# Optimization experiments

Measured on AMD Instinct MI355X. Metric: run time of the kernel, lower is better.

## Reference

```python
import jax, jax.numpy as jnp
import numpy as np

K_DIM = 1024
HEADS = 16
D_K = K_DIM // HEADS


def setup_inputs() -> dict:
    key = jax.random.key(0)
    ks = jax.random.split(key, 6)
    b, t, k = 4, 1024, K_DIM
    scale = 1.0 / np.sqrt(k)
    return {
        "x": jax.random.normal(ks[0], (b, t, k), dtype=jnp.float32),
        "Wq": jax.random.normal(ks[1], (k, k), dtype=jnp.float32) * scale,
        "Wk": jax.random.normal(ks[2], (k, k), dtype=jnp.float32) * scale,
        "Wv": jax.random.normal(ks[3], (k, k), dtype=jnp.float32) * scale,
        "Wo": jax.random.normal(ks[4], (k, k), dtype=jnp.float32) * scale,
        "bo": jax.random.normal(ks[5], (k,), dtype=jnp.float32) * 0.01,
    }


def reference(x, Wq, Wk, Wv, Wo, bo):
    b, t, k = x.shape
    h, d_k = HEADS, D_K
    # Linear(k,k) applies x @ W.T; project then split heads -> [b, h, t, d_k]
    Q = (x @ Wq.T).reshape(b, t, h, d_k).transpose(0, 2, 1, 3)
    Kh = (x @ Wk.T).reshape(b, t, h, d_k).transpose(0, 2, 1, 3)
    V = (x @ Wv.T).reshape(b, t, h, d_k).transpose(0, 2, 1, 3)
    scores = jnp.einsum("bhqd,bhkd->bhqk", Q, Kh) / jnp.sqrt(jnp.float32(d_k))
    attn = jax.nn.softmax(scores, axis=-1)
    out = jnp.einsum("bhqk,bhkd->bhqd", attn, V)
    out = out.transpose(0, 2, 1, 3).reshape(b, t, k)
    return out @ Wo.T + bo
```

## Files before the change

### kernel.cpp

```cpp
#include <hip/hip_runtime.h>
#include <hip/hip_bf16.h>

typedef __attribute__((ext_vector_type(4))) float f32x4;
typedef __attribute__((ext_vector_type(8))) short short8;

#define B_   4
#define T_   1024
#define H_   16
#define DK_  64
#define KDIM 1024

#define QSCALE 0.18033688011112042f

__device__ __forceinline__ unsigned short f2bf(float f){
  union { float f; unsigned int u; } a; a.f = f;
  unsigned int u = a.u;
  return (unsigned short)((u + 0x7FFFu + ((u >> 16) & 1u)) >> 16);
}

__device__ __forceinline__ unsigned short f2bf_rn(float f){
  union { __hip_bfloat16 h; unsigned short u; } cv;
  cv.h = __float2bfloat16(f);
  return cv.u;
}

__device__ __forceinline__ void gload16(const void* g, void* l){
  __builtin_amdgcn_global_load_lds(
      (const __attribute__((address_space(1))) unsigned int*)g,
      (__attribute__((address_space(3))) unsigned int*)l,
      16, 0, 0);
}

__global__ __launch_bounds__(256) void convert5(
    const float* __restrict__ x,  const float* __restrict__ wq,
    const float* __restrict__ wk, const float* __restrict__ wv,
    const float* __restrict__ wo,
    short* __restrict__ xb,  short* __restrict__ wqb,
    short* __restrict__ wkb, short* __restrict__ wvb, short* __restrict__ wob)
{
  int i = blockIdx.x * 256 + threadIdx.x;
  const float* s; short* d; int off;
  if (i < (1 << 20)) { s = x; d = xb; off = i; }
  else {
    int j = i - (1 << 20);
    int w = j >> 18;
    off = j & ((1 << 18) - 1);
    s = (w == 0) ? wq : (w == 1) ? wk : (w == 2) ? wv : wo;
    d = (w == 0) ? wqb : (w == 1) ? wkb : (w == 2) ? wvb : wob;
  }
  float4 v = ((const float4*)s)[off];
  ushort4 o;
  o.x = f2bf(v.x); o.y = f2bf(v.y); o.z = f2bf(v.z); o.w = f2bf(v.w);
  ((ushort4*)d)[off] = o;
}

__device__ __forceinline__ void gemm2_core(
    const short* __restrict__ A, const short* __restrict__ W,
    int m0, int n0, short* As, short* Bs, f32x4 acc[4][4])
{
  const int tid = threadIdx.x, wv = tid >> 6, lane = tid & 63;
  const int lr = lane & 15, lq = lane >> 4;
  const int wr = wv >> 1, wc = wv & 1;
  const int swz = (lr & 7) << 3;
  const int r8 = lane >> 3;
  const int c8 = ((lane & 7) * 8) ^ (r8 * 8);

#pragma unroll
  for (int m = 0; m < 4; ++m)
#pragma unroll
    for (int n = 0; n < 4; ++n) acc[m][n] = (f32x4){0.f, 0.f, 0.f, 0.f};

  auto stage = [&](int buf, int kt) {
    const int k0 = kt * 64;
#pragma unroll
    for (int i = 0; i < 4; ++i) {
      const int r = (wv * 4 + i) * 8 + r8;
      gload16(A + (size_t)(m0 + r) * KDIM + k0 + c8, As + buf * 8192 + (wv * 4 + i) * 512);
      gload16(W + (size_t)(n0 + r) * KDIM + k0 + c8, Bs + buf * 8192 + (wv * 4 + i) * 512);
    }
  };

  stage(0, 0);
  asm volatile("s_waitcnt vmcnt(0)" ::: "memory");
  __builtin_amdgcn_s_barrier();

  int buf = 0;
  for (int kt = 0; kt < 16; ++kt) {
    if (kt < 15) stage(buf ^ 1, kt + 1);
    const short* Ab = As + buf * 8192;
    const short* Bb = Bs + buf * 8192;
#pragma unroll
    for (int kk = 0; kk < 2; ++kk) {
      short8 af[4], bfv[4];
#pragma unroll
      for (int m = 0; m < 4; ++m)
        af[m] = *(const short8*)(Ab + (wr * 64 + m * 16 + lr) * 64 + ((kk * 32 + lq * 8) ^ swz));
#pragma unroll
      for (int n = 0; n < 4; ++n)
        bfv[n] = *(const short8*)(Bb + (wc * 64 + n * 16 + lr) * 64 + ((kk * 32 + lq * 8) ^ swz));
      __builtin_amdgcn_s_setprio(1);
#pragma unroll
      for (int m = 0; m < 4; ++m)
#pragma unroll
        for (int n = 0; n < 4; ++n)
          acc[m][n] = __builtin_amdgcn_mfma_f32_16x16x32_bf16(af[m], bfv[n], acc[m][n], 0, 0, 0);
      __builtin_amdgcn_s_setprio(0);
    }
    asm volatile("s_waitcnt vmcnt(0)" ::: "memory");
    __builtin_amdgcn_s_barrier();
    buf ^= 1;
  }
}

__global__ __launch_bounds__(256, 2) void gemm2_qkv(
    const short* __restrict__ xb,
    const short* __restrict__ Wqb, const short* __restrict__ Wkb, const short* __restrict__ Wvb,
    short* __restrict__ Qb, short* __restrict__ Kb, short* __restrict__ VTb)
{
  __shared__ __align__(16) short As[2 * 8192];
  __shared__ __align__(16) short Bs[2 * 8192];
  const int bid = blockIdx.x;
  const int wgid = (bid & 7) * 96 + (bid >> 3);
  const int mx = wgid / 24, inner = wgid % 24;
  const int wsel = inner >> 3;
  const int m0 = mx * 128, n0 = (inner & 7) * 128;
  const short* W = (wsel == 0) ? Wqb : (wsel == 1) ? Wkb : Wvb;

  f32x4 acc[4][4];
  gemm2_core(xb, W, m0, n0, As, Bs, acc);

  const int tid = threadIdx.x, lane = tid & 63, wv = tid >> 6;
  const int lr = lane & 15, lq = lane >> 4, wr = wv >> 1, wc = wv & 1;
  if (wsel < 2) {
    short* O = wsel ? Kb : Qb;
    const float sc = wsel ? 1.0f : QSCALE;
#pragma unroll
    for (int m = 0; m < 4; ++m)
#pragma unroll
      for (int n = 0; n < 4; ++n)
#pragma unroll
        for (int j = 0; j < 4; ++j) {
          int row = m0 + wr * 64 + m * 16 + lq * 4 + j;
          int col = n0 + wc * 64 + n * 16 + lr;
          O[(size_t)row * KDIM + col] = (short)f2bf(acc[m][n][j] * sc);
        }
  } else {
#pragma unroll
    for (int m = 0; m < 4; ++m)
#pragma unroll
      for (int n = 0; n < 4; ++n) {
        int row = m0 + wr * 64 + m * 16 + lq * 4;
        int col = n0 + wc * 64 + n * 16 + lr;
        int b = row >> 10, t = row & 1023, h = col >> 6, d = col & 63;
        ushort4 v;
        v.x = f2bf(acc[m][n][0]); v.y = f2bf(acc[m][n][1]);
        v.z = f2bf(acc[m][n][2]); v.w = f2bf(acc[m][n][3]);
        *(ushort4*)&VTb[(size_t)((b * 16 + h) * 64 + d) * 1024 + t] = v;
      }
  }
}

__global__ __launch_bounds__(256, 2) void gemm2_out(
    const short* __restrict__ AOb, const short* __restrict__ Wob,
    const float* __restrict__ bias, float* __restrict__ out)
{
  __shared__ __align__(16) short As[2 * 8192];
  __shared__ __align__(16) short Bs[2 * 8192];
  const int bid = blockIdx.x;
  const int wgid = (bid & 7) * 32 + (bid >> 3);
  const int mx = wgid >> 3, ny = wgid & 7;
  const int m0 = mx * 128, n0 = ny * 128;

  f32x4 acc[4][4];
  gemm2_core(AOb, Wob, m0, n0, As, Bs, acc);

  const int tid = threadIdx.x, lane = tid & 63, wv = tid >> 6;
  const int lr = lane & 15, lq = lane >> 4, wr = wv >> 1, wc = wv & 1;
#pragma unroll
  for (int m = 0; m < 4; ++m)
#pragma unroll
    for (int n = 0; n < 4; ++n) {
      int col = n0 + wc * 64 + n * 16 + lr;
      float bv = bias[col];
#pragma unroll
      for (int j = 0; j < 4; ++j) {
        int row = m0 + wr * 64 + m * 16 + lq * 4 + j;
        out[(size_t)row * KDIM + col] = acc[m][n][j] + bv;
      }
    }
}

__global__ __launch_bounds__(256) void attn_kern(
    const short* __restrict__ Qb, const short* __restrict__ Kb,
    const short* __restrict__ VTb, short* __restrict__ AOb)
{
  __shared__ __align__(16) short kl[2][64 * 64];
  __shared__ __align__(16) short vl[2][64 * 64];
  __shared__ __align__(16) short pl[4][16 * 64];
  const int flat = blockIdx.y * 16 + blockIdx.x;
  const int wg = (flat & 7) * 128 + (flat >> 3);
  const int bh = wg >> 4, b = bh >> 4, h = bh & 15;
  const int q0 = (wg & 15) * 64;
  const int tid = threadIdx.x, wv = tid >> 6, lane = tid & 63;
  const int lr = lane & 15, lq = lane >> 4;

  const short* Qrow = Qb + (size_t)(b * T_ + q0 + wv * 16 + lr) * KDIM + h * DK_;
  short8 qf0 = *(const short8*)(Qrow + lq * 8);
  short8 qf1 = *(const short8*)(Qrow + 32 + lq * 8);

  const short* Kbase = Kb + (size_t)(b * T_) * KDIM + h * DK_;
  const short* Vbase = VTb + (size_t)(bh * DK_) * 1024;

  const int srow = tid >> 3, scol = (tid & 7) * 8;

  auto stage = [&](int buf, int kv0) {
#pragma unroll
    for (int p = 0; p < 2; ++p) {
      const int r = p * 32 + srow;
      gload16(Kbase + (size_t)(kv0 + r) * KDIM + (scol ^ ((r & 7) << 3)),
              &kl[buf][p * 2048 + wv * 512]);
    }
#pragma unroll
    for (int p = 0; p < 2; ++p) {
      const int r = p * 32 + srow;
      gload16(Vbase + (size_t)r * 1024 + kv0 + (scol ^ ((r & 7) << 3)),
              &vl[buf][p * 2048 + wv * 512]);
    }
  };

  f32x4 oacc[4];
#pragma unroll
  for (int i = 0; i < 4; ++i) oacc[i] = (f32x4){0.f, 0.f, 0.f, 0.f};
  float m_r = -1e30f, l_r = 0.f;
  const int swq = (lr & 7) << 3;
  short* plw = pl[wv];

  int cur = 0;
  stage(0, 0);
  __syncthreads();

  for (int kt = 0; kt < 16; ++kt) {
    if (kt < 15) stage(cur ^ 1, (kt + 1) * 64);

    f32x4 s[4];
#pragma unroll
    for (int nt = 0; nt < 4; ++nt) {
      const int kr = nt * 16 + lr;
      const int sw = (kr & 7) << 3;
      short8 kf0 = *(const short8*)&kl[cur][kr * 64 + ((lq * 8) ^ sw)];
      short8 kf1 = *(const short8*)&kl[cur][kr * 64 + ((32 + lq * 8) ^ sw)];
      f32x4 z = (f32x4){0.f, 0.f, 0.f, 0.f};
      z = __builtin_amdgcn_mfma_f32_16x16x32_bf16(kf0, qf0, z, 0, 0, 0);
      s[nt] = __builtin_amdgcn_mfma_f32_16x16x32_bf16(kf1, qf1, z, 0, 0, 0);
    }

    float mx;
    {
      float a0 = fmaxf(fmaxf(s[0][0], s[0][1]), fmaxf(s[0][2], s[0][3]));
      float a1 = fmaxf(fmaxf(s[1][0], s[1][1]), fmaxf(s[1][2], s[1][3]));
      float a2 = fmaxf(fmaxf(s[2][0], s[2][1]), fmaxf(s[2][2], s[2][3]));
      float a3 = fmaxf(fmaxf(s[3][0], s[3][1]), fmaxf(s[3][2], s[3][3]));
      mx = fmaxf(fmaxf(a0, a1), fmaxf(a2, a3));
    }
    mx = fmaxf(mx, __shfl_xor(mx, 16));
    mx = fmaxf(mx, __shfl_xor(mx, 32));
    if (!__all(mx <= m_r + 8.f)) {
      const float mn = fmaxf(m_r, mx);
      const float al = exp2f(m_r - mn);
      l_r *= al;
#pragma unroll
      for (int nt = 0; nt < 4; ++nt)
#pragma unroll
        for (int j = 0; j < 4; ++j) oacc[nt][j] *= al;
      m_r = mn;
    }
    float rs = 0.f;
#pragma unroll
    for (int nt = 0; nt < 4; ++nt)
#pragma unroll
      for (int j = 0; j < 4; ++j) {
        float e = exp2f(s[nt][j] - m_r);
        s[nt][j] = e;
        rs += e;
      }
    rs += __shfl_xor(rs, 16);
    rs += __shfl_xor(rs, 32);
    l_r += rs;

#pragma unroll
    for (int nt = 0; nt < 4; ++nt) {
      f32x4 v = s[nt];
      ushort4 u;
      u.x = f2bf_rn(v[0]); u.y = f2bf_rn(v[1]);
      u.z = f2bf_rn(v[2]); u.w = f2bf_rn(v[3]);
      *(ushort4*)&plw[lr * 64 + ((nt * 16 + lq * 4) ^ swq)] = u;
    }
    asm volatile("s_waitcnt lgkmcnt(0)" ::: "memory");
    short8 pf0 = *(const short8*)&plw[lr * 64 + ((lq * 8) ^ swq)];
    short8 pf1 = *(const short8*)&plw[lr * 64 + ((32 + lq * 8) ^ swq)];
#pragma unroll
    for (int ntd = 0; ntd < 4; ++ntd) {
      const int vr = ntd * 16 + lr;
      const int sw = (vr & 7) << 3;
      short8 vf0 = *(const short8*)&vl[cur][vr * 64 + ((lq * 8) ^ sw)];
      short8 vf1 = *(const short8*)&vl[cur][vr * 64 + ((32 + lq * 8) ^ sw)];
      oacc[ntd] = __builtin_amdgcn_mfma_f32_16x16x32_bf16(vf0, pf0, oacc[ntd], 0, 0, 0);
      oacc[ntd] = __builtin_amdgcn_mfma_f32_16x16x32_bf16(vf1, pf1, oacc[ntd], 0, 0, 0);
    }
    __syncthreads();
    cur ^= 1;
  }

  const float inv = 1.0f / l_r;
#pragma unroll
  for (int nt = 0; nt < 4; ++nt) {
    ushort4 u;
    u.x = f2bf_rn(oacc[nt][0] * inv);
    u.y = f2bf_rn(oacc[nt][1] * inv);
    u.z = f2bf_rn(oacc[nt][2] * inv);
    u.w = f2bf_rn(oacc[nt][3] * inv);
    *(ushort4*)&AOb[(size_t)(b * T_ + q0 + wv * 16 + lr) * KDIM + h * DK_ + nt * 16 + lq * 4] = u;
  }
}

extern "C" void kernel_launch(void* const* d_in, const int* in_sizes, int n_in,
                              void* d_out, int out_size, void* d_ws, size_t ws_size,
                              hipStream_t stream) {
  const float* x  = (const float*)d_in[0];
  const float* Wq = (const float*)d_in[1];
  const float* Wk = (const float*)d_in[2];
  const float* Wv = (const float*)d_in[3];
  const float* Wo = (const float*)d_in[4];
  const float* bo = (const float*)d_in[5];

  short* ws = (short*)d_ws;
  short* xb  = ws;
  short* Wqb = ws + 4194304;
  short* Wkb = ws + 5242880;
  short* Wvb = ws + 6291456;
  short* Wob = ws + 7340032;
  short* Qb  = ws + 8388608;
  short* Kb  = ws + 12582912;
  short* VTb = ws + 16777216;
  short* AOb = ws + 20971520;

  convert5<<<8192, 256, 0, stream>>>(x, Wq, Wk, Wv, Wo, xb, Wqb, Wkb, Wvb, Wob);
  gemm2_qkv<<<768, 256, 0, stream>>>(xb, Wqb, Wkb, Wvb, Qb, Kb, VTb);
  attn_kern<<<dim3(16, 64), 256, 0, stream>>>(Qb, Kb, VTb, AOb);
  gemm2_out<<<256, 256, 0, stream>>>(AOb, Wob, bo, (float*)d_out);
}
```

Baseline: 186.9 us.

## Vectorize GEMM epilogue stores via swapped MFMA operands; double query rows per attention wave

The GEMM core is templated so that for Q/K and output projections the MFMA operands are swapped, making each lane hold 4 consecutive columns and allowing vectorized ushort4/float4 stores instead of scalar strided stores. The attention kernel now processes 32 query rows per wave (128 per block, 512 blocks), so every K/V tile loaded into LDS is reused twice, halving K/V global traffic per query. This raises register pressure (doubled accumulators and scores) and halves block count, which may reduce occupancy.

After: 189.5 us. No clear change (+1.4%).

```diff
diff --git a/kernel.cpp b/kernel.cpp
--- a/kernel.cpp
+++ b/kernel.cpp
@@ -54,6 +54,7 @@
   ((ushort4*)d)[off] = o;
 }
 
+template<bool SWAP>
 __device__ __forceinline__ void gemm2_core(
     const short* __restrict__ A, const short* __restrict__ W,
     int m0, int n0, short* As, short* Bs, f32x4 acc[4][4])
@@ -102,8 +103,12 @@
 #pragma unroll
       for (int m = 0; m < 4; ++m)
 #pragma unroll
-        for (int n = 0; n < 4; ++n)
-          acc[m][n] = __builtin_amdgcn_mfma_f32_16x16x32_bf16(af[m], bfv[n], acc[m][n], 0, 0, 0);
+        for (int n = 0; n < 4; ++n) {
+          if constexpr (SWAP)
+            acc[m][n] = __builtin_amdgcn_mfma_f32_16x16x32_bf16(bfv[n], af[m], acc[m][n], 0, 0, 0);
+          else
+            acc[m][n] = __builtin_amdgcn_mfma_f32_16x16x32_bf16(af[m], bfv[n], acc[m][n], 0, 0, 0);
+        }
       __builtin_amdgcn_s_setprio(0);
     }
     asm volatile("s_waitcnt vmcnt(0)" ::: "memory");
@@ -126,25 +131,29 @@
   const int m0 = mx * 128, n0 = (inner & 7) * 128;
   const short* W = (wsel == 0) ? Wqb : (wsel == 1) ? Wkb : Wvb;
 
-  f32x4 acc[4][4];
-  gemm2_core(xb, W, m0, n0, As, Bs, acc);
-
   const int tid = threadIdx.x, lane = tid & 63, wv = tid >> 6;
   const int lr = lane & 15, lq = lane >> 4, wr = wv >> 1, wc = wv & 1;
+
   if (wsel < 2) {
+    f32x4 acc[4][4];
+    gemm2_core<true>(xb, W, m0, n0, As, Bs, acc);
     short* O = wsel ? Kb : Qb;
     const float sc = wsel ? 1.0f : QSCALE;
 #pragma unroll
-    for (int m = 0; m < 4; ++m)
-#pragma unroll
-      for (int n = 0; n < 4; ++n)
-#pragma unroll
-        for (int j = 0; j < 4; ++j) {
-          int row = m0 + wr * 64 + m * 16 + lq * 4 + j;
-          int col = n0 + wc * 64 + n * 16 + lr;
-          O[(size_t)row * KDIM + col] = (short)f2bf(acc[m][n][j] * sc);
-        }
+    for (int m = 0; m < 4; ++m) {
+      const int row = m0 + wr * 64 + m * 16 + lr;
+#pragma unroll
+      for (int n = 0; n < 4; ++n) {
+        const int colb = n0 + wc * 64 + n * 16 + lq * 4;
+        ushort4 u;
+        u.x = f2bf(acc[m][n][0] * sc); u.y = f2bf(acc[m][n][1] * sc);
+        u.z = f2bf(acc[m][n][2] * sc); u.w = f2bf(acc[m][n][3] * sc);
+        *(ushort4*)&O[(size_t)row * KDIM + colb] = u;
+      }
+    }
   } else {
+    f32x4 acc[4][4];
+    gemm2_core<false>(xb, W, m0, n0, As, Bs, acc);
 #pragma unroll
     for (int m = 0; m < 4; ++m)
 #pragma unroll
@@ -172,22 +181,23 @@
   const int m0 = mx * 128, n0 = ny * 128;
 
   f32x4 acc[4][4];
-  gemm2_core(AOb, Wob, m0, n0, As, Bs, acc);
+  gemm2_core<true>(AOb, Wob, m0, n0, As, Bs, acc);
 
   const int tid = threadIdx.x, lane = tid & 63, wv = tid >> 6;
   const int lr = lane & 15, lq = lane >> 4, wr = wv >> 1, wc = wv & 1;
 #pragma unroll
-  for (int m = 0; m < 4; ++m)
-#pragma unroll
-    for (int n = 0; n < 4; ++n) {
-      int col = n0 + wc * 64 + n * 16 + lr;
-      float bv = bias[col];
-#pragma unroll
-      for (int j = 0; j < 4; ++j) {
-        int row = m0 + wr * 64 + m * 16 + lq * 4 + j;
-        out[(size_t)row * KDIM + col] = acc[m][n][j] + bv;
-      }
-    }
+  for (int n = 0; n < 4; ++n) {
+    const int colb = n0 + wc * 64 + n * 16 + lq * 4;
+    const float4 bv = *(const float4*)&bias[colb];
+#pragma unroll
+    for (int m = 0; m < 4; ++m) {
+      const int row = m0 + wr * 64 + m * 16 + lr;
+      float4 o;
+      o.x = acc[m][n][0] + bv.x; o.y = acc[m][n][1] + bv.y;
+      o.z = acc[m][n][2] + bv.z; o.w = acc[m][n][3] + bv.w;
+      *(float4*)&out[(size_t)row * KDIM + colb] = o;
+    }
+  }
 }
 
 __global__ __launch_bounds__(256) void attn_kern(
@@ -196,17 +206,21 @@
 {
   __shared__ __align__(16) short kl[2][64 * 64];
   __shared__ __align__(16) short vl[2][64 * 64];
-  __shared__ __align__(16) short pl[4][16 * 64];
-  const int flat = blockIdx.y * 16 + blockIdx.x;
-  const int wg = (flat & 7) * 128 + (flat >> 3);
-  const int bh = wg >> 4, b = bh >> 4, h = bh & 15;
-  const int q0 = (wg & 15) * 64;
+  __shared__ __align__(16) short pl[8][16 * 64];
+  const int flat = blockIdx.x;
+  const int wg = (flat & 7) * 64 + (flat >> 3);
+  const int bh = wg >> 3, b = bh >> 4, h = bh & 15;
+  const int q0 = (wg & 7) * 128;
   const int tid = threadIdx.x, wv = tid >> 6, lane = tid & 63;
   const int lr = lane & 15, lq = lane >> 4;
 
-  const short* Qrow = Qb + (size_t)(b * T_ + q0 + wv * 16 + lr) * KDIM + h * DK_;
-  short8 qf0 = *(const short8*)(Qrow + lq * 8);
-  short8 qf1 = *(const short8*)(Qrow + 32 + lq * 8);
+  short8 qf[2][2];
+#pragma unroll
+  for (int g = 0; g < 2; ++g) {
+    const short* Qrow = Qb + (size_t)(b * T_ + q0 + wv * 32 + g * 16 + lr) * KDIM + h * DK_;
+    qf[g][0] = *(const short8*)(Qrow + lq * 8);
+    qf[g][1] = *(const short8*)(Qrow + 32 + lq * 8);
+  }
 
   const short* Kbase = Kb + (size_t)(b * T_) * KDIM + h * DK_;
   const short* Vbase = VTb + (size_t)(bh * DK_) * 1024;
@@ -228,12 +242,13 @@
     }
   };
 
-  f32x4 oacc[4];
-#pragma unroll
-  for (int i = 0; i < 4; ++i) oacc[i] = (f32x4){0.f, 0.f, 0.f, 0.f};
-  float m_r = -1e30f, l_r = 0.f;
+  f32x4 oacc[2][4];
+#pragma unroll
+  for (int g = 0; g < 2; ++g)
+#pragma unroll
+    for (int i = 0; i < 4; ++i) oacc[g][i] = (f32x4){0.f, 0.f, 0.f, 0.f};
+  float m_r[2] = {-1e30f, -1e30f}, l_r[2] = {0.f, 0.f};
   const int swq = (lr & 7) << 3;
-  short* plw = pl[wv];
 
   int cur = 0;
   stage(0, 0);
@@ -242,84 +257,107 @@
   for (int kt = 0; kt < 16; ++kt) {
     if (kt < 15) stage(cur ^ 1, (kt + 1) * 64);
 
-    f32x4 s[4];
+    f32x4 s[2][4];
 #pragma unroll
     for (int nt = 0; nt < 4; ++nt) {
       const int kr = nt * 16 + lr;
       const int sw = (kr & 7) << 3;
       short8 kf0 = *(const short8*)&kl[cur][kr * 64 + ((lq * 8) ^ sw)];
       short8 kf1 = *(const short8*)&kl[cur][kr * 64 + ((32 + lq * 8) ^ sw)];
-      f32x4 z = (f32x4){0.f, 0.f, 0.f, 0.f};
-      z = __builtin_amdgcn_mfma_f32_16x16x32_bf16(kf0, qf0, z, 0, 0, 0);
-      s[nt] = __builtin_amdgcn_mfma_f32_16x16x32_bf16(kf1, qf1, z, 0, 0, 0);
-    }
-
-    float mx;
-    {
-      float a0 = fmaxf(fmaxf(s[0][0], s[0][1]), fmaxf(s[0][2], s[0][3]));
-      float a1 = fmaxf(fmaxf(s[1][0], s[1][1]), fmaxf(s[1][2], s[1][3]));
-      float a2 = fmaxf(fmaxf(s[2][0], s[2][1]), fmaxf(s[2][2], s[2][3]));
-      float a3 = fmaxf(fmaxf(s[3][0], s[3][1]), fmaxf(s[3][2], s[3][3]));
-      mx = fmaxf(fmaxf(a0, a1), fmaxf(a2, a3));
-    }
-    mx = fmaxf(mx, __shfl_xor(mx, 16));
-    mx = fmaxf(mx, __shfl_xor(mx, 32));
-    if (!__all(mx <= m_r + 8.f)) {
-      const float mn = fmaxf(m_r, mx);
-      const float al = exp2f(m_r - mn);
-      l_r *= al;
+#pragma unroll
+      for (int g = 0; g < 2; ++g) {
+        f32x4 z = (f32x4){0.f, 0.f, 0.f, 0.f};
+        z = __builtin_amdgcn_mfma_f32_16x16x32_bf16(kf0, qf[g][0], z, 0, 0, 0);
+        s[g][nt] = __builtin_amdgcn_mfma_f32_16x16x32_bf16(kf1, qf[g][1], z, 0, 0, 0);
+      }
+    }
+
+#pragma unroll
+    for (int g = 0; g < 2; ++g) {
+      float mx;
+      {
+        float a0 = fmaxf(fmaxf(s[g][0][0], s[g][0][1]), fmaxf(s[g][0][2], s[g][0][3]));
+        float a1 = fmaxf(fmaxf(s[g][1][0], s[g][1][1]), fmaxf(s[g][1][2], s[g][1][3]));
+        float a2 = fmaxf(fmaxf(s[g][2][0], s[g][2][1]), fmaxf(s[g][2][2], s[g][2][3]));
+        float a3 = fmaxf(fmaxf(s[g][3][0], s[g][3][1]), fmaxf(s[g][3][2], s[g][3][3]));
+        mx = fmaxf(fmaxf(a0, a1), fmaxf(a2, a3));
+      }
+      mx = fmaxf(mx, __shfl_xor(mx, 16));
+      mx = fmaxf(mx, __shfl_xor(mx, 32));
+      if (!__all(mx <= m_r[g] + 8.f)) {
+        const float mn = fmaxf(m_r[g], mx);
+        const float al = exp2f(m_r[g] - mn);
+        l_r[g] *= al;
+#pragma unroll
+        for (int nt = 0; nt < 4; ++nt)
+#pragma unroll
+          for (int j = 0; j < 4; ++j) oacc[g][nt][j] *= al;
+        m_r[g] = mn;
+      }
+      float rs = 0.f;
 #pragma unroll
       for (int nt = 0; nt < 4; ++nt)
 #pragma unroll
-        for (int j = 0; j < 4; ++j) oacc[nt][j] *= al;
-      m_r = mn;
-    }
-    float rs = 0.f;
-#pragma unroll
-    for (int nt = 0; nt < 4; ++nt)
-#pragma unroll
-      for (int j = 0; j < 4; ++j) {
-        float e = exp2f(s[nt][j] - m_r);
-        s[nt][j] = e;
-        rs += e;
-      }
-    rs += __shfl_xor(rs, 16);
-    rs += __shfl_xor(rs, 32);
-    l_r += rs;
-
-#pragma unroll
-    for (int nt = 0; nt < 4; ++nt) {
-      f32x4 v = s[nt];
-      ushort4 u;
-      u.x = f2bf_rn(v[0]); u.y = f2bf_rn(v[1]);
-      u.z = f2bf_rn(v[2]); u.w = f2bf_rn(v[3]);
-      *(ushort4*)&plw[lr * 64 + ((nt * 16 + lq * 4) ^ swq)] = u;
+        for (int j = 0; j < 4; ++j) {
+          float e = exp2f(s[g][nt][j] - m_r[g]);
+          s[g][nt][j] = e;
+          rs += e;
+        }
+      rs += __shfl_xor(rs, 16);
+      rs += __shfl_xor(rs, 32);
+      l_r[g] += rs;
+    }
+
+#pragma unroll
+    for (int g = 0; g < 2; ++g) {
+      short* plw = pl[wv * 2 + g];
+#pragma unroll
+      for (int nt = 0; nt < 4; ++nt) {
+        ushort4 u;
+        u.x = f2bf_rn(s[g][nt][0]); u.y = f2bf_rn(s[g][nt][1]);
+        u.z = f2bf_rn(s[g][nt][2]); u.w = f2bf_rn(s[g][nt][3]);
+        *(ushort4*)&plw[lr * 64 + ((nt * 16 + lq * 4) ^ swq)] = u;
+      }
     }
     asm volatile("s_waitcnt lgkmcnt(0)" ::: "memory");
-    short8 pf0 = *(const short8*)&plw[lr * 64 + ((lq * 8) ^ swq)];
-    short8 pf1 = *(const short8*)&plw[lr * 64 + ((32 + lq * 8) ^ swq)];
+
+    short8 pf[2][2];
+#pragma unroll
+    for (int g = 0; g < 2; ++g) {
+      short* plw = pl[wv * 2 + g];
+      pf[g][0] = *(const short8*)&plw[lr * 64 + ((lq * 8) ^ swq)];
+      pf[g][1] = *(const short8*)&plw[lr * 64 + ((32 + lq * 8) ^ swq)];
+    }
+
 #pragma unroll
     for (int ntd = 0; ntd < 4; ++ntd) {
       const int vr = ntd * 16 + lr;
       const int sw = (vr & 7) << 3;
       short8 vf0 = *(const short8*)&vl[cur][vr * 64 + ((lq * 8) ^ sw)];
       short8 vf1 = *(const short8*)&vl[cur][vr * 64 + ((32 + lq * 8) ^ sw)];
-      oacc[ntd] = __builtin_amdgcn_mfma_f32_16x16x32_bf16(vf0, pf0, oacc[ntd], 0, 0, 0);
-      oacc[ntd] = __builtin_amdgcn_mfma_f32_16x16x32_bf16(vf1, pf1, oacc[ntd], 0, 0, 0);
+#pragma unroll
+      for (int g = 0; g < 2; ++g) {
+        oacc[g][ntd] = __builtin_amdgcn_mfma_f32_16x16x32_bf16(vf0, pf[g][0], oacc[g][ntd], 0, 0, 0);
+        oacc[g][ntd] = __builtin_amdgcn_mfma_f32_16x16x32_bf16(vf1, pf[g][1], oacc[g][ntd], 0, 0, 0);
+      }
     }
     __syncthreads();
     cur ^= 1;
   }
 
-  const float inv = 1.0f / l_r;
-#pragma unroll
-  for (int nt = 0; nt < 4; ++nt) {
-    ushort4 u;
-    u.x = f2bf_rn(oacc[nt][0] * inv);
-    u.y = f2bf_rn(oacc[nt][1] * inv);
-    u.z = f2bf_rn(oacc[nt][2] * inv);
-    u.w = f2bf_rn(oacc[nt][3] * inv);
-    *(ushort4*)&AOb[(size_t)(b * T_ + q0 + wv * 16 + lr) * KDIM + h * DK_ + nt * 16 + lq * 4] = u;
+#pragma unroll
+  for (int g = 0; g < 2; ++g) {
+    const float inv = 1.0f / l_r[g];
+    const size_t rowb = (size_t)(b * T_ + q0 + wv * 32 + g * 16 + lr) * KDIM + h * DK_;
+#pragma unroll
+    for (int nt = 0; nt < 4; ++nt) {
+      ushort4 u;
+      u.x = f2bf_rn(oacc[g][nt][0] * inv);
+      u.y = f2bf_rn(oacc[g][nt][1] * inv);
+      u.z = f2bf_rn(oacc[g][nt][2] * inv);
+      u.w = f2bf_rn(oacc[g][nt][3] * inv);
+      *(ushort4*)&AOb[rowb + nt * 16 + lq * 4] = u;
+    }
   }
 }
 
@@ -346,6 +384,6 @@
 
   convert5<<<8192, 256, 0, stream>>>(x, Wq, Wk, Wv, Wo, xb, Wqb, Wkb, Wvb, Wob);
   gemm2_qkv<<<768, 256, 0, stream>>>(xb, Wqb, Wkb, Wvb, Qb, Kb, VTb);
-  attn_kern<<<dim3(16, 64), 256, 0, stream>>>(Qb, Kb, VTb, AOb);
+  attn_kern<<<512, 256, 0, stream>>>(Qb, Kb, VTb, AOb);
   gemm2_out<<<256, 256, 0, stream>>>(AOb, Wob, bo, (float*)d_out);
 }
```

## Keep P in registers via permuted K rows and vectorize GEMM epilogue stores

Applied to the files above, without the earlier changes.

The attention kernel now reads K rows in a permuted order so each lane's score accumulator already matches the B-operand layout of the P·V MFMA. P is packed to bf16 in registers with v_cvt_pk_bf16_f32, which removes the per-wave LDS round trip and its waitcnt; the LDS swizzle is adjusted to suit the new access pattern. The Q/K projection and output GEMMs swap MFMA operands so each lane holds consecutive columns, turning scalar epilogue stores into 8- and 16-byte vector stores. This adds some index arithmetic and changes the rounding path for the attention output conversion.

Result: no change. 186.2 us (-0.4%).

```diff
diff --git a/kernel.cpp b/kernel.cpp
--- a/kernel.cpp
+++ b/kernel.cpp
@@ -18,10 +18,10 @@
   return (unsigned short)((u + 0x7FFFu + ((u >> 16) & 1u)) >> 16);
 }
 
-__device__ __forceinline__ unsigned short f2bf_rn(float f){
-  union { __hip_bfloat16 h; unsigned short u; } cv;
-  cv.h = __float2bfloat16(f);
-  return cv.u;
+__device__ __forceinline__ unsigned int cvtpk_bf16(float lo, float hi){
+  unsigned int r;
+  asm("v_cvt_pk_bf16_f32 %0, %1, %2" : "=v"(r) : "v"(lo), "v"(hi));
+  return r;
 }
 
 __device__ __forceinline__ void gload16(const void* g, void* l){
@@ -54,6 +54,7 @@
   ((ushort4*)d)[off] = o;
 }
 
+template<bool SWAP>
 __device__ __forceinline__ void gemm2_core(
     const short* __restrict__ A, const short* __restrict__ W,
     int m0, int n0, short* As, short* Bs, f32x4 acc[4][4])
@@ -102,8 +103,12 @@
 #pragma unroll
       for (int m = 0; m < 4; ++m)
 #pragma unroll
-        for (int n = 0; n < 4; ++n)
-          acc[m][n] = __builtin_amdgcn_mfma_f32_16x16x32_bf16(af[m], bfv[n], acc[m][n], 0, 0, 0);
+        for (int n = 0; n < 4; ++n) {
+          if constexpr (SWAP)
+            acc[m][n] = __builtin_amdgcn_mfma_f32_16x16x32_bf16(bfv[n], af[m], acc[m][n], 0, 0, 0);
+          else
+            acc[m][n] = __builtin_amdgcn_mfma_f32_16x16x32_bf16(af[m], bfv[n], acc[m][n], 0, 0, 0);
+        }
       __builtin_amdgcn_s_setprio(0);
     }
     asm volatile("s_waitcnt vmcnt(0)" ::: "memory");
@@ -126,25 +131,29 @@
   const int m0 = mx * 128, n0 = (inner & 7) * 128;
   const short* W = (wsel == 0) ? Wqb : (wsel == 1) ? Wkb : Wvb;
 
-  f32x4 acc[4][4];
-  gemm2_core(xb, W, m0, n0, As, Bs, acc);
-
   const int tid = threadIdx.x, lane = tid & 63, wv = tid >> 6;
   const int lr = lane & 15, lq = lane >> 4, wr = wv >> 1, wc = wv & 1;
+
   if (wsel < 2) {
+    f32x4 acc[4][4];
+    gemm2_core<true>(xb, W, m0, n0, As, Bs, acc);
     short* O = wsel ? Kb : Qb;
     const float sc = wsel ? 1.0f : QSCALE;
 #pragma unroll
-    for (int m = 0; m < 4; ++m)
-#pragma unroll
-      for (int n = 0; n < 4; ++n)
-#pragma unroll
-        for (int j = 0; j < 4; ++j) {
-          int row = m0 + wr * 64 + m * 16 + lq * 4 + j;
-          int col = n0 + wc * 64 + n * 16 + lr;
-          O[(size_t)row * KDIM + col] = (short)f2bf(acc[m][n][j] * sc);
-        }
+    for (int m = 0; m < 4; ++m) {
+      const int row = m0 + wr * 64 + m * 16 + lr;
+#pragma unroll
+      for (int n = 0; n < 4; ++n) {
+        const int colb = n0 + wc * 64 + n * 16 + lq * 4;
+        ushort4 u;
+        u.x = f2bf(acc[m][n][0] * sc); u.y = f2bf(acc[m][n][1] * sc);
+        u.z = f2bf(acc[m][n][2] * sc); u.w = f2bf(acc[m][n][3] * sc);
+        *(ushort4*)&O[(size_t)row * KDIM + colb] = u;
+      }
+    }
   } else {
+    f32x4 acc[4][4];
+    gemm2_core<false>(xb, W, m0, n0, As, Bs, acc);
 #pragma unroll
     for (int m = 0; m < 4; ++m)
 #pragma unroll
@@ -172,22 +181,23 @@
   const int m0 = mx * 128, n0 = ny * 128;
 
   f32x4 acc[4][4];
-  gemm2_core(AOb, Wob, m0, n0, As, Bs, acc);
+  gemm2_core<true>(AOb, Wob, m0, n0, As, Bs, acc);
 
   const int tid = threadIdx.x, lane = tid & 63, wv = tid >> 6;
   const int lr = lane & 15, lq = lane >> 4, wr = wv >> 1, wc = wv & 1;
 #pragma unroll
-  for (int m = 0; m < 4; ++m)
-#pragma unroll
-    for (int n = 0; n < 4; ++n) {
-      int col = n0 + wc * 64 + n * 16 + lr;
-      float bv = bias[col];
-#pragma unroll
-      for (int j = 0; j < 4; ++j) {
-        int row = m0 + wr * 64 + m * 16 + lq * 4 + j;
-        out[(size_t)row * KDIM + col] = acc[m][n][j] + bv;
-      }
-    }
+  for (int n = 0; n < 4; ++n) {
+    const int colb = n0 + wc * 64 + n * 16 + lq * 4;
+    const float4 bv = *(const float4*)&bias[colb];
+#pragma unroll
+    for (int m = 0; m < 4; ++m) {
+      const int row = m0 + wr * 64 + m * 16 + lr;
+      float4 o;
+      o.x = acc[m][n][0] + bv.x; o.y = acc[m][n][1] + bv.y;
+      o.z = acc[m][n][2] + bv.z; o.w = acc[m][n][3] + bv.w;
+      *(float4*)&out[(size_t)row * KDIM + colb] = o;
+    }
+  }
 }
 
 __global__ __launch_bounds__(256) void attn_kern(
@@ -196,8 +206,7 @@
 {
   __shared__ __align__(16) short kl[2][64 * 64];
   __shared__ __align__(16) short vl[2][64 * 64];
-  __shared__ __align__(16) short pl[4][16 * 64];
-  const int flat = blockIdx.y * 16 + blockIdx.x;
+  const int flat = blockIdx.x;
   const int wg = (flat & 7) * 128 + (flat >> 3);
   const int bh = wg >> 4, b = bh >> 4, h = bh & 15;
   const int q0 = (wg & 15) * 64;
@@ -213,17 +222,19 @@
 
   const int srow = tid >> 3, scol = (tid & 7) * 8;
 
+  auto sw = [](int r) { return ((r & 7) ^ ((r & 8) >> 1)) << 3; };
+
   auto stage = [&](int buf, int kv0) {
 #pragma unroll
     for (int p = 0; p < 2; ++p) {
       const int r = p * 32 + srow;
-      gload16(Kbase + (size_t)(kv0 + r) * KDIM + (scol ^ ((r & 7) << 3)),
+      gload16(Kbase + (size_t)(kv0 + r) * KDIM + (scol ^ sw(r)),
               &kl[buf][p * 2048 + wv * 512]);
     }
 #pragma unroll
     for (int p = 0; p < 2; ++p) {
       const int r = p * 32 + srow;
-      gload16(Vbase + (size_t)r * 1024 + kv0 + (scol ^ ((r & 7) << 3)),
+      gload16(Vbase + (size_t)r * 1024 + kv0 + (scol ^ sw(r)),
               &vl[buf][p * 2048 + wv * 512]);
     }
   };
@@ -232,8 +243,8 @@
 #pragma unroll
   for (int i = 0; i < 4; ++i) oacc[i] = (f32x4){0.f, 0.f, 0.f, 0.f};
   float m_r = -1e30f, l_r = 0.f;
-  const int swq = (lr & 7) << 3;
-  short* plw = pl[wv];
+
+  const int koff = 8 * (lr >> 2) + (lr & 3);
 
   int cur = 0;
   stage(0, 0);
@@ -243,12 +254,13 @@
     if (kt < 15) stage(cur ^ 1, (kt + 1) * 64);
 
     f32x4 s[4];
+    const int offs[4] = {0, 4, 32, 36};
 #pragma unroll
     for (int nt = 0; nt < 4; ++nt) {
-      const int kr = nt * 16 + lr;
-      const int sw = (kr & 7) << 3;
-      short8 kf0 = *(const short8*)&kl[cur][kr * 64 + ((lq * 8) ^ sw)];
-      short8 kf1 = *(const short8*)&kl[cur][kr * 64 + ((32 + lq * 8) ^ sw)];
+      const int kr = koff + offs[nt];
+      const int swr = sw(kr);
+      short8 kf0 = *(const short8*)&kl[cur][kr * 64 + ((lq * 8) ^ swr)];
+      short8 kf1 = *(const short8*)&kl[cur][kr * 64 + ((32 + lq * 8) ^ swr)];
       f32x4 z = (f32x4){0.f, 0.f, 0.f, 0.f};
       z = __builtin_amdgcn_mfma_f32_16x16x32_bf16(kf0, qf0, z, 0, 0, 0);
       s[nt] = __builtin_amdgcn_mfma_f32_16x16x32_bf16(kf1, qf1, z, 0, 0, 0);
@@ -287,25 +299,24 @@
     rs += __shfl_xor(rs, 32);
     l_r += rs;
 
-#pragma unroll
-    for (int nt = 0; nt < 4; ++nt) {
-      f32x4 v = s[nt];
-      ushort4 u;
-      u.x = f2bf_rn(v[0]); u.y = f2bf_rn(v[1]);
-      u.z = f2bf_rn(v[2]); u.w = f2bf_rn(v[3]);
-      *(ushort4*)&plw[lr * 64 + ((nt * 16 + lq * 4) ^ swq)] = u;
-    }
-    asm volatile("s_waitcnt lgkmcnt(0)" ::: "memory");
-    short8 pf0 = *(const short8*)&plw[lr * 64 + ((lq * 8) ^ swq)];
-    short8 pf1 = *(const short8*)&plw[lr * 64 + ((32 + lq * 8) ^ swq)];
+    union { unsigned int u[4]; short8 v; } pk0, pk1;
+    pk0.u[0] = cvtpk_bf16(s[0][0], s[0][1]);
+    pk0.u[1] = cvtpk_bf16(s[0][2], s[0][3]);
+    pk0.u[2] = cvtpk_bf16(s[1][0], s[1][1]);
+    pk0.u[3] = cvtpk_bf16(s[1][2], s[1][3]);
+    pk1.u[0] = cvtpk_bf16(s[2][0], s[2][1]);
+    pk1.u[1] = cvtpk_bf16(s[2][2], s[2][3]);
+    pk1.u[2] = cvtpk_bf16(s[3][0], s[3][1]);
+    pk1.u[3] = cvtpk_bf16(s[3][2], s[3][3]);
+
 #pragma unroll
     for (int ntd = 0; ntd < 4; ++ntd) {
       const int vr = ntd * 16 + lr;
-      const int sw = (vr & 7) << 3;
-      short8 vf0 = *(const short8*)&vl[cur][vr * 64 + ((lq * 8) ^ sw)];
-      short8 vf1 = *(const short8*)&vl[cur][vr * 64 + ((32 + lq * 8) ^ sw)];
-      oacc[ntd] = __builtin_amdgcn_mfma_f32_16x16x32_bf16(vf0, pf0, oacc[ntd], 0, 0, 0);
-      oacc[ntd] = __builtin_amdgcn_mfma_f32_16x16x32_bf16(vf1, pf1, oacc[ntd], 0, 0, 0);
+      const int swr = sw(vr);
+      short8 vf0 = *(const short8*)&vl[cur][vr * 64 + ((lq * 8) ^ swr)];
+      short8 vf1 = *(const short8*)&vl[cur][vr * 64 + ((32 + lq * 8) ^ swr)];
+      oacc[ntd] = __builtin_amdgcn_mfma_f32_16x16x32_bf16(vf0, pk0.v, oacc[ntd], 0, 0, 0);
+      oacc[ntd] = __builtin_amdgcn_mfma_f32_16x16x32_bf16(vf1, pk1.v, oacc[ntd], 0, 0, 0);
     }
     __syncthreads();
     cur ^= 1;
@@ -315,10 +326,10 @@
 #pragma unroll
   for (int nt = 0; nt < 4; ++nt) {
     ushort4 u;
-    u.x = f2bf_rn(oacc[nt][0] * inv);
-    u.y = f2bf_rn(oacc[nt][1] * inv);
-    u.z = f2bf_rn(oacc[nt][2] * inv);
-    u.w = f2bf_rn(oacc[nt][3] * inv);
+    u.x = f2bf(oacc[nt][0] * inv);
+    u.y = f2bf(oacc[nt][1] * inv);
+    u.z = f2bf(oacc[nt][2] * inv);
+    u.w = f2bf(oacc[nt][3] * inv);
     *(ushort4*)&AOb[(size_t)(b * T_ + q0 + wv * 16 + lr) * KDIM + h * DK_ + nt * 16 + lq * 4] = u;
   }
 }
@@ -346,6 +357,6 @@
 
   convert5<<<8192, 256, 0, stream>>>(x, Wq, Wk, Wv, Wo, xb, Wqb, Wkb, Wvb, Wob);
   gemm2_qkv<<<768, 256, 0, stream>>>(xb, Wqb, Wkb, Wvb, Qb, Kb, VTb);
-  attn_kern<<<dim3(16, 64), 256, 0, stream>>>(Qb, Kb, VTb, AOb);
+  attn_kern<<<1024, 256, 0, stream>>>(Qb, Kb, VTb, AOb);
   gemm2_out<<<256, 256, 0, stream>>>(AOb, Wob, bo, (float*)d_out);
 }
```
